# Performance work log

Measured on AMD Instinct MI355X. Metric: run time of the kernel, lower is better.

The kernel has to match this reference:

```python
import jax, jax.numpy as jnp
import numpy as np

# Inside algorithm for a binary TreeCRF over a complete binary tree in heap
# layout: node i has children 2i+1 and 2i+2; level of size n starts at index
# n-1. Leaves are the last (n_nodes+1)//2 entries of `emissions`.
#
# Original per-node math:
#   inside[p] = logsumexp_{i,j}( em[p] + trans[p,i] + left[i] + trans[p,j] + right[j] )
# which factorizes exactly as
#   inside[p] = em[p] + logsumexp_i(trans[p,i]+left[i]) + logsumexp_j(trans[p,j]+right[j])


def setup_inputs() -> dict:
    key = jax.random.key(0)
    k1, k2 = jax.random.split(key)
    n_leaves = 131072  # 2**17
    n_nodes = 2 * n_leaves - 1  # 262143
    L = 32
    emissions = jax.random.normal(k1, (n_nodes, L), dtype=jnp.float32)
    trans = jax.random.normal(k2, (L, L), dtype=jnp.float32)
    return {"emissions": emissions, "trans": trans}


def _child_contrib(trans, child):
    # child: [n, L] inside scores of children; trans: [L, L]
    # returns [n, L]: logsumexp_c(trans[p, c] + child[:, c])
    return jax.nn.logsumexp(trans[None, :, :] + child[:, None, :], axis=2)


def reference(emissions, trans):
    n_nodes = emissions.shape[0]
    n_leaves = (n_nodes + 1) // 2
    # leaf inside scores are just the leaf emissions
    scores = emissions[n_leaves - 1:]  # [n_leaves, L]
    level = n_leaves // 2
    while level >= 1:
        # children of node (level-1)+k are scores[2k] (left) and scores[2k+1] (right)
        left = scores[0::2]   # [level, L]
        right = scores[1::2]  # [level, L]
        em = emissions[level - 1: 2 * level - 1]  # [level, L]
        scores = em + _child_contrib(trans, left) + _child_contrib(trans, right)
        level //= 2
    return scores[0]  # root inside score, [L]
```

## Files before the change

### kernel.cpp

```cpp
#include <hip/hip_runtime.h>


typedef float f32x4 __attribute__((ext_vector_type(4)));
typedef short s16x8 __attribute__((ext_vector_type(8)));
typedef short s16x4 __attribute__((ext_vector_type(4)));

__device__ __forceinline__ short f2bf(float f) {
    unsigned u = __builtin_bit_cast(unsigned, f);
    unsigned r = (u + 0x7fffu + ((u >> 16) & 1u)) >> 16;
    return (short)r;
}

#define MSTEP(mask) { float4 o; o.x=__shfl_xor(r.x,mask); o.y=__shfl_xor(r.y,mask); \
                      o.z=__shfl_xor(r.z,mask); o.w=__shfl_xor(r.w,mask); \
                      r.x=fmaxf(r.x,o.x); r.y=fmaxf(r.y,o.y); \
                      r.z=fmaxf(r.z,o.z); r.w=fmaxf(r.w,o.w); }

template <int NT, int LEVELS>
__device__ __forceinline__ void run_tree(
    const int t, int Wp, int boff, const int b,
    const float* __restrict__ gchild,
    const float* __restrict__ em,
    const s16x8 a0, const s16x8 a1,
    short* __restrict__ CA, float* __restrict__ MA,
    short* __restrict__ CB, float* __restrict__ MB,
    float* __restrict__ gout)
{
    const int NC0 = 1 << LEVELS;
    for (int u = t; u < NC0 * 8; u += NT) {
        int ql = u >> 3, k = u & 7;
        float4 x = ((const float4*)(gchild + (size_t)ql * 32))[k];
        float4 r = x;
        MSTEP(1) MSTEP(2) MSTEP(4)
        float m = fmaxf(fmaxf(r.x, r.y), fmaxf(r.z, r.w));
        s16x4 w;
        w[0] = f2bf(__expf(x.x - m)); w[1] = f2bf(__expf(x.y - m));
        w[2] = f2bf(__expf(x.z - m)); w[3] = f2bf(__expf(x.w - m));
        *((s16x4*)(CA + ql * 32 + k * 4)) = w;
        if (k == 0) MA[ql] = m;
    }
    __syncthreads();

    short* Cs = CA; float* Ms = MA;
    short* Cd = CB; float* Md = MB;
    const int lane = t & 63, wv = t >> 6, nw = NT / 64;
    const int ql = lane & 15, kg = lane >> 4;
    int nc = NC0;
    for (int l = 0; l < LEVELS; ++l) {
        int nqt = (nc >= 16) ? (nc >> 4) : 1;
        for (int qt = wv; qt < nqt; qt += nw) {
            int q = qt * 16 + ql;
            bool valid = q < nc;
            s16x8 bf = *((const s16x8*)(Cs + q * 32 + kg * 8));
            f32x4 d0 = {0.f, 0.f, 0.f, 0.f};
            f32x4 d1 = {0.f, 0.f, 0.f, 0.f};
            d0 = __builtin_amdgcn_mfma_f32_16x16x32_bf16(a0, bf, d0, 0, 0, 0);
            d1 = __builtin_amdgcn_mfma_f32_16x16x32_bf16(a1, bf, d1, 0, 0, 0);
            float mq = Ms[q];
            int p = qt * 8 + (ql >> 1);
            size_t node = (size_t)(Wp - 1) + (size_t)boff * b + p;
            const float4 e0 = *((const float4*)(em + node * 32 + kg * 4));
            const float4 e1 = *((const float4*)(em + node * 32 + 16 + kg * 4));
            float v0[4], v1[4];
#pragma unroll
        for (int r2 = 0; r2 < 4; ++r2) {
                float t0 = mq + __logf(d0[r2]);
                float t1 = mq + __logf(d1[r2]);
                v0[r2] = t0 + __shfl_xor(t0, 1);
                v1[r2] = t1 + __shfl_xor(t1, 1);
            }
            v0[0] += e0.x; v0[1] += e0.y; v0[2] += e0.z; v0[3] += e0.w;
            v1[0] += e1.x; v1[1] += e1.y; v1[2] += e1.z; v1[3] += e1.w;
            if (l == LEVELS - 1) {
                if (ql == 0) {
                    float4 o0 = {v0[0], v0[1], v0[2], v0[3]};
                    float4 o1 = {v1[0], v1[1], v1[2], v1[3]};
                    *((float4*)(gout + kg * 4)) = o0;
                    *((float4*)(gout + 16 + kg * 4)) = o1;
                }
            } else {
                float m2 = fmaxf(fmaxf(fmaxf(v0[0], v0[1]), fmaxf(v0[2], v0[3])),
                                 fmaxf(fmaxf(v1[0], v1[1]), fmaxf(v1[2], v1[3])));
                m2 = fmaxf(m2, __shfl_xor(m2, 16));
                m2 = fmaxf(m2, __shfl_xor(m2, 32));
                if (valid && !(ql & 1)) {
                    s16x4 w0, w1;
                    w0[0] = f2bf(__expf(v0[0] - m2)); w0[1] = f2bf(__expf(v0[1] - m2));
                    w0[2] = f2bf(__expf(v0[2] - m2)); w0[3] = f2bf(__expf(v0[3] - m2));
                    w1[0] = f2bf(__expf(v1[0] - m2)); w1[1] = f2bf(__expf(v1[1] - m2));
                    w1[2] = f2bf(__expf(v1[2] - m2)); w1[3] = f2bf(__expf(v1[3] - m2));
                    *((s16x4*)(Cd + p * 32 + kg * 4)) = w0;
                    *((s16x4*)(Cd + p * 32 + 16 + kg * 4)) = w1;
                    if (kg == 0) Md[p] = m2;
                }
            }
        }
        __syncthreads();
        short* tc = Cs; Cs = Cd; Cd = tc;
        float* tm = Ms; Ms = Md; Md = tm;
        nc >>= 1; Wp >>= 1; boff >>= 1;
    }
}

__device__ __forceinline__ void load_afrag(const float* __restrict__ trans,
                                           int row, int kg, s16x8* a)
{
#pragma unroll
    for (int j = 0; j < 8; ++j)
        (*a)[j] = f2bf(__expf(trans[row * 32 + kg * 8 + j]));
}

__global__ __launch_bounds__(512) void treecrf_bottom(
    const float* __restrict__ em, const float* __restrict__ trans,
    float* __restrict__ out512, int n_leaves)
{
    __shared__ short CA[256 * 32];
    __shared__ short CB[128 * 32];
    __shared__ float MA[256];
    __shared__ float MB[128];
    int t = threadIdx.x, b = blockIdx.x;
    int ql = t & 15, kg = (t & 63) >> 4;
    s16x8 a0, a1;
    load_afrag(trans, ql, kg, &a0);
    load_afrag(trans, ql + 16, kg, &a1);
    run_tree<512, 8>(t, n_leaves >> 1, 128, b,
                     em + (size_t)(n_leaves - 1 + 256 * b) * 32, em, a0, a1,
                     CA, MA, CB, MB, out512 + (size_t)b * 32);
}

__global__ __launch_bounds__(1024) void treecrf_top(
    const float* __restrict__ g512, const float* __restrict__ em,
    const float* __restrict__ trans, float* __restrict__ out_root)
{
    __shared__ short CA[512 * 32];
    __shared__ short CB[256 * 32];
    __shared__ float MA[512];
    __shared__ float MB[256];
    int t = threadIdx.x;
    int ql = t & 15, kg = (t & 63) >> 4;
    s16x8 a0, a1;
    load_afrag(trans, ql, kg, &a0);
    load_afrag(trans, ql + 16, kg, &a1);
    run_tree<1024, 9>(t, 256, 0, 0, g512, em, a0, a1,
                      CA, MA, CB, MB, out_root);
}

extern "C" void kernel_launch(void* const* d_in, const int* in_sizes, int n_in,
                              void* d_out, int out_size, void* d_ws, size_t ws_size,
                              hipStream_t stream)
{
    const float* em = (const float*)d_in[0];
    const float* trans = (const float*)d_in[1];
    int n_nodes = in_sizes[0] / 32;
    int n_leaves = (n_nodes + 1) / 2;
    int blocksA = n_leaves / 256;

    float* out512 = (float*)d_ws;
    treecrf_bottom<<<dim3(blocksA), dim3(512), 0, stream>>>(em, trans, out512,
                                                            n_leaves);
    treecrf_top<<<dim3(1), dim3(1024), 0, stream>>>(out512, em, trans,
                                                    (float*)d_out);
}
```

Measured before the change: 98.95 us.

## Fuse bottom and top tree kernels using a last-block atomic counter

Merges the two kernel launches into one. Each block reduces its 256-leaf subtree, then increments a global counter, and the last block to finish runs the top 9 levels over the 512 partial results. This removes the second kernel launch and the gap between the two kernels, at the cost of an added memset launch. Shared memory per block grows to fit the top tree, which may lower occupancy in the bottom phase, and the top phase now runs with 512 threads instead of 1024.

```diff
diff --git a/kernel.cpp b/kernel.cpp
--- a/kernel.cpp
+++ b/kernel.cpp
@@ -63,7 +63,7 @@
             const float4 e1 = *((const float4*)(em + node * 32 + 16 + kg * 4));
             float v0[4], v1[4];
 #pragma unroll
-        for (int r2 = 0; r2 < 4; ++r2) {
+            for (int r2 = 0; r2 < 4; ++r2) {
                 float t0 = mq + __logf(d0[r2]);
                 float t1 = mq + __logf(d1[r2]);
                 v0[r2] = t0 + __shfl_xor(t0, 1);
@@ -110,39 +110,36 @@
         (*a)[j] = f2bf(__expf(trans[row * 32 + kg * 8 + j]));
 }
 
-__global__ __launch_bounds__(512) void treecrf_bottom(
+__global__ __launch_bounds__(512) void treecrf_fused(
     const float* __restrict__ em, const float* __restrict__ trans,
-    float* __restrict__ out512, int n_leaves)
+    float* __restrict__ out512, int* __restrict__ counter,
+    float* __restrict__ out_root, int n_leaves, int nbm1)
 {
-    __shared__ short CA[256 * 32];
-    __shared__ short CB[128 * 32];
-    __shared__ float MA[256];
-    __shared__ float MB[128];
+    __shared__ short CA[512 * 32];
+    __shared__ short CB[256 * 32];
+    __shared__ float MA[512];
+    __shared__ float MB[256];
+    __shared__ int last_flag;
     int t = threadIdx.x, b = blockIdx.x;
     int ql = t & 15, kg = (t & 63) >> 4;
     s16x8 a0, a1;
     load_afrag(trans, ql, kg, &a0);
     load_afrag(trans, ql + 16, kg, &a1);
+
     run_tree<512, 8>(t, n_leaves >> 1, 128, b,
                      em + (size_t)(n_leaves - 1 + 256 * b) * 32, em, a0, a1,
                      CA, MA, CB, MB, out512 + (size_t)b * 32);
-}
 
-__global__ __launch_bounds__(1024) void treecrf_top(
-    const float* __restrict__ g512, const float* __restrict__ em,
-    const float* __restrict__ trans, float* __restrict__ out_root)
-{
-    __shared__ short CA[512 * 32];
-    __shared__ short CB[256 * 32];
-    __shared__ float MA[512];
-    __shared__ float MB[256];
-    int t = threadIdx.x;
-    int ql = t & 15, kg = (t & 63) >> 4;
-    s16x8 a0, a1;
-    load_afrag(trans, ql, kg, &a0);
-    load_afrag(trans, ql + 16, kg, &a1);
-    run_tree<1024, 9>(t, 256, 0, 0, g512, em, a0, a1,
-                      CA, MA, CB, MB, out_root);
+    if (t == 0) {
+        __threadfence();
+        last_flag = (atomicAdd(counter, 1) == nbm1);
+    }
+    __syncthreads();
+    if (!last_flag) return;
+    __threadfence();
+
+    run_tree<512, 9>(t, 256, 0, 0, out512, em, a0, a1,
+                     CA, MA, CB, MB, out_root);
 }
 
 extern "C" void kernel_launch(void* const* d_in, const int* in_sizes, int n_in,
@@ -153,11 +150,12 @@
     const float* trans = (const float*)d_in[1];
     int n_nodes = in_sizes[0] / 32;
     int n_leaves = (n_nodes + 1) / 2;
-    int blocksA = n_leaves / 256;
+    int blocks = n_leaves / 256;
 
     float* out512 = (float*)d_ws;
-    treecrf_bottom<<<dim3(blocksA), dim3(512), 0, stream>>>(em, trans, out512,
-                                                            n_leaves);
-    treecrf_top<<<dim3(1), dim3(1024), 0, stream>>>(out512, em, trans,
-                                                    (float*)d_out);
+    int* counter = (int*)((char*)d_ws + 512 * 32 * sizeof(float));
+
+    hipMemsetAsync(counter, 0, sizeof(int), stream);
+    treecrf_fused<<<dim3(blocks), dim3(512), 0, stream>>>(
+        em, trans, out512, counter, (float*)d_out, n_leaves, blocks - 1);
 }
```

Result: slower. 109.7 us (+10.9%).
